# Performance work log

Hardware: AMD Instinct MI355X
Metric: run time of the kernel (lower is better)

Reference implementation:

```python
import jax, jax.numpy as jnp
import numpy as np

N = 50000   # nodes
E = 800000  # edges (before self-loops)
DIN = 128
H, C = 4, 32
HC = H * C  # 128
DE = 3      # edge feature dim
G = 64      # graphs in batch
HID = 32
DOUT = 1
LN_EPS = 1e-5


def setup_inputs() -> dict:
    key = jax.random.key(0)
    ks = iter(jax.random.split(key, 64))
    def nrm(shape, s=0.1):
        return jax.random.normal(next(ks), shape, dtype=jnp.float32) * s
    inp = {}
    inp["x"] = jax.random.normal(next(ks), (N, DIN), dtype=jnp.float32)
    inp["edge_index"] = jax.random.randint(next(ks), (2, E), 0, N, dtype=jnp.int32)
    inp["batch"] = jnp.sort(jax.random.randint(next(ks), (N,), 0, G, dtype=jnp.int32))
    inp["edge_attr"] = jax.random.normal(next(ks), (E, DE), dtype=jnp.float32)
    # GATv2 layers: layer0 in=DIN(128); layers 1,2 in=HC(128)
    for l, din in enumerate([DIN, HC, HC]):
        inp[f"Wl{l}"] = nrm((HC, din)); inp[f"bl{l}"] = jnp.zeros((HC,), jnp.float32)
        inp[f"Wr{l}"] = nrm((HC, din)); inp[f"br{l}"] = jnp.zeros((HC,), jnp.float32)
        inp[f"We{l}"] = nrm((HC, DE))
        inp[f"att{l}"] = nrm((H, C))
        inp[f"bo{l}"] = jnp.zeros((HC,), jnp.float32)
    for l in range(2):
        inp[f"ln{l}_g"] = jnp.ones((HC,), jnp.float32)
        inp[f"ln{l}_b"] = jnp.zeros((HC,), jnp.float32)
    # post-processing MLP: 128->32->32->32->1
    inp["pw1"] = nrm((HID, HC)); inp["pb1"] = jnp.zeros((HID,), jnp.float32)
    inp["pw2"] = nrm((HID, HID)); inp["pb2"] = jnp.zeros((HID,), jnp.float32)
    inp["pw3"] = nrm((HID, HID)); inp["pb3"] = jnp.zeros((HID,), jnp.float32)
    inp["pw4"] = nrm((DOUT, HID)); inp["pb4"] = jnp.zeros((DOUT,), jnp.float32)
    return inp


def _gat_layer(x, src, dst, eattr, Wl, bl, Wr, br, We, att, bo):
    # GATv2Conv (concat heads). x_l from lin_l -> source, x_r from lin_r -> target.
    xl = (x @ Wl.T + bl).reshape(-1, H, C)
    xr = (x @ Wr.T + br).reshape(-1, H, C)
    e = (eattr @ We.T).reshape(-1, H, C)
    m = jax.nn.leaky_relu(xl[src] + xr[dst] + e, negative_slope=0.2)  # [E',H,C]
    s = jnp.einsum('ehc,hc->eh', m, att)                              # [E',H]
    smax = jax.ops.segment_max(s, dst, num_segments=N)
    ex = jnp.exp(s - smax[dst])
    den = jax.ops.segment_sum(ex, dst, num_segments=N)
    alpha = ex / (den[dst] + 1e-16)
    out = jax.ops.segment_sum(alpha[:, :, None] * xl[src], dst, num_segments=N)
    return out.reshape(-1, HC) + bo


def _ln(x, g, b):
    mu = jnp.mean(x, axis=-1, keepdims=True)
    var = jnp.mean((x - mu) ** 2, axis=-1, keepdims=True)
    return (x - mu) * jax.lax.rsqrt(var + LN_EPS) * g + b


def _forward(x, edge_attr, edge_index, batch, p):
    src0, dst0 = edge_index[0], edge_index[1]
    # PyG add_self_loops with fill_value='mean': per-dst-node mean of edge_attr
    cnt = jax.ops.segment_sum(jnp.ones((E,), jnp.float32), dst0, num_segments=N)
    loop_attr = jax.ops.segment_sum(edge_attr, dst0, num_segments=N) / jnp.maximum(cnt, 1.0)[:, None]
    ar = jnp.arange(N, dtype=src0.dtype)
    src = jnp.concatenate([src0, ar]); dst = jnp.concatenate([dst0, ar])
    ea = jnp.concatenate([edge_attr, loop_attr], axis=0)
    embedding = x
    for l in range(3):
        x = _gat_layer(x, src, dst, ea, p[f"Wl{l}"], p[f"bl{l}"], p[f"Wr{l}"],
                       p[f"br{l}"], p[f"We{l}"], p[f"att{l}"], p[f"bo{l}"])
        embedding = x
        x = jax.nn.relu(x)  # dropout inactive (eval)
        if l != 2:
            x = _ln(x, p[f"ln{l}_g"], p[f"ln{l}_b"])
    pooled = jax.ops.segment_max(x, batch, num_segments=G)
    pooled = jnp.where(jnp.isfinite(pooled), pooled, 0.0)
    h = jax.nn.relu(pooled @ p["pw1"].T + p["pb1"])
    h = jax.nn.relu(h @ p["pw2"].T + p["pb2"])
    h = jax.nn.relu(h @ p["pw3"].T + p["pb3"])
    out = h @ p["pw4"].T + p["pb4"]
    return embedding, out


def reference(x, edge_index, batch, edge_attr,
              Wl0, bl0, Wr0, br0, We0, att0, bo0,
              Wl1, bl1, Wr1, br1, We1, att1, bo1,
              Wl2, bl2, Wr2, br2, We2, att2, bo2,
              ln0_g, ln0_b, ln1_g, ln1_b,
              pw1, pb1, pw2, pb2, pw3, pb3, pw4, pb4):
    p = dict(Wl0=Wl0, bl0=bl0, Wr0=Wr0, br0=br0, We0=We0, att0=att0, bo0=bo0,
             Wl1=Wl1, bl1=bl1, Wr1=Wr1, br1=br1, We1=We1, att1=att1, bo1=bo1,
             Wl2=Wl2, bl2=bl2, Wr2=Wr2, br2=br2, We2=We2, att2=att2, bo2=bo2,
             ln0_g=ln0_g, ln0_b=ln0_b, ln1_g=ln1_g, ln1_b=ln1_b,
             pw1=pw1, pb1=pb1, pw2=pw2, pb2=pb2, pw3=pw3, pb3=pb3, pw4=pw4, pb4=pb4)
    return _forward(x, edge_attr, edge_index, batch, p)
```

## Files before the change

### kernel.cpp

```cpp
#include <hip/hip_runtime.h>
#include <math.h>


#define LN_EPS 1e-5f
#define LOG2E 1.44269504088896340736f

typedef short bf16x8 __attribute__((ext_vector_type(8)));
typedef float f32x4 __attribute__((ext_vector_type(4)));

static __device__ __forceinline__ unsigned short f2bf(float f) {
  unsigned int u = __float_as_uint(f);
  u += 0x7fffu + ((u >> 16) & 1u);
  return (unsigned short)(u >> 16);
}

static __device__ __forceinline__ float dpp_sum8(float v) {
  int x;
  x = __builtin_amdgcn_update_dpp(0, __float_as_int(v), 0x0B1, 0xf, 0xf, true);
  v += __int_as_float(x);
  x = __builtin_amdgcn_update_dpp(0, __float_as_int(v), 0x04E, 0xf, 0xf, true);
  v += __int_as_float(x);
  x = __builtin_amdgcn_update_dpp(0, __float_as_int(v), 0x141, 0xf, 0xf, true);
  v += __int_as_float(x);
  return v;
}


__global__ void k_degree(const int* __restrict__ ei, int* __restrict__ cnt, int E) {
  int e = (blockIdx.x * blockDim.x + threadIdx.x) * 4;
  if (e + 3 < E) {
    int4 d = *(const int4*)&ei[E + e];
    atomicAdd(&cnt[d.x], 1);
    atomicAdd(&cnt[d.y], 1);
    atomicAdd(&cnt[d.z], 1);
    atomicAdd(&cnt[d.w], 1);
  } else {
    int lim = min(e + 4, E);
    for (; e < lim; ++e) atomicAdd(&cnt[ei[E + e]], 1);
  }
}

__global__ void k_scan1(const int* __restrict__ cnt, int* __restrict__ bsum, int N) {
  __shared__ int sh[256];
  int t = threadIdx.x;
  int n = blockIdx.x * 256 + t;
  sh[t] = (n < N) ? (cnt[n] + 1) : 0;
  __syncthreads();
  for (int s = 128; s > 0; s >>= 1) {
    if (t < s) sh[t] += sh[t + s];
    __syncthreads();
  }
  if (t == 0) bsum[blockIdx.x] = sh[0];
}

__global__ void k_scan2(int* __restrict__ bsum, int* __restrict__ offs, int nb, int total, int N) {
  __shared__ int sh[256];
  int t = threadIdx.x;
  int v = (t < nb) ? bsum[t] : 0;
  sh[t] = v;
  __syncthreads();
  for (int d = 1; d < 256; d <<= 1) {
    int add = (t >= d) ? sh[t - d] : 0;
    __syncthreads();
    sh[t] += add;
    __syncthreads();
  }
  if (t < nb) bsum[t] = sh[t] - v;
  if (t == 0) offs[N] = total;
}

__global__ void k_scan3(const int* __restrict__ cnt, const int* __restrict__ bsum,
                        int* __restrict__ offs, int* __restrict__ cursor, int N) {
  __shared__ int sh[256];
  int t = threadIdx.x;
  int n = blockIdx.x * 256 + t;
  int v = (n < N) ? (cnt[n] + 1) : 0;
  sh[t] = v;
  __syncthreads();
  for (int d = 1; d < 256; d <<= 1) {
    int add = (t >= d) ? sh[t - d] : 0;
    __syncthreads();
    sh[t] += add;
    __syncthreads();
  }
  if (n < N) {
    int o = bsum[blockIdx.x] + sh[t] - v;
    offs[n] = o;
    cursor[n] = o;
  }
}

__global__ void k_scatter(const int* __restrict__ ei, const float* __restrict__ ea,
                          int* __restrict__ cursor, float4* __restrict__ e4, int E) {
  int e = blockIdx.x * blockDim.x + threadIdx.x;
  if (e >= E) return;
  int s = ei[e];
  int d = ei[E + e];
  int pos = atomicAdd(&cursor[d], 1);
  float4 r;
  r.x = ea[e * 3 + 0];
  r.y = ea[e * 3 + 1];
  r.z = ea[e * 3 + 2];
  r.w = __int_as_float(s * 256);
  e4[pos] = r;
}

__global__ void k_selfloop(const int* __restrict__ offs, float4* __restrict__ e4, int N) {
  int n = blockIdx.x * blockDim.x + threadIdx.x;
  if (n >= N) return;
  int beg = offs[n], last = offs[n + 1] - 1;
  float s0 = 0.f, s1 = 0.f, s2 = 0.f;
  for (int p = beg; p < last; ++p) {
    float4 v = e4[p];
    s0 += v.x;
    s1 += v.y;
    s2 += v.z;
  }
  float invc = 1.0f / fmaxf((float)(last - beg), 1.0f);
  float4 r;
  r.x = s0 * invc;
  r.y = s1 * invc;
  r.z = s2 * invc;
  r.w = __int_as_float(n * 256);
  e4[last] = r;
}


__global__ void k_convx(const float* __restrict__ x, unsigned short* __restrict__ xb, int n) {
  int i = (blockIdx.x * blockDim.x + threadIdx.x) * 4;
  if (i >= n) return;
  float4 v = *(const float4*)&x[i];
  ushort4 o;
  o.x = f2bf(v.x); o.y = f2bf(v.y); o.z = f2bf(v.z); o.w = f2bf(v.w);
  *(ushort4*)&xb[i] = o;
}

__global__ void k_convW(const float* __restrict__ w0, const float* __restrict__ w1,
                        const float* __restrict__ w2, const float* __restrict__ w3,
                        const float* __restrict__ w4, const float* __restrict__ w5,
                        unsigned short* __restrict__ dst) {
  const float* srcs[6] = {w0, w1, w2, w3, w4, w5};
  const float* s = srcs[blockIdx.y];
  int i = blockIdx.x * 256 + threadIdx.x;
  dst[(size_t)blockIdx.y * 16384 + i] = f2bf(s[i]);
}

__global__ __launch_bounds__(256) void k_gemm_mfma(const unsigned short* __restrict__ xb,
                                                   const unsigned short* __restrict__ Wb,
                                                   const float* __restrict__ bl, const float* __restrict__ br,
                                                   unsigned short* __restrict__ xlb,
                                                   unsigned short* __restrict__ xrb, int N) {
  int wave = threadIdx.x >> 6;
  int lane = threadIdx.x & 63;
  int which = blockIdx.y;
  const unsigned short* W = Wb + (size_t)which * 16384;
  const float* bias = which ? br : bl;
  unsigned short* out = which ? xrb : xlb;

  int row0 = (blockIdx.x * 4 + wave) * 16;
  if (row0 >= N) return;
  int m = lane & 15;
  int q = lane >> 4;

  int arow = row0 + m;
  if (arow >= N) arow = N - 1;
  const unsigned short* xrow = xb + (size_t)arow * 128 + q * 8;

  bf16x8 afrag[4];
#pragma unroll
  for (int kt = 0; kt < 4; ++kt) afrag[kt] = *(const bf16x8*)(xrow + kt * 32);

  f32x4 acc[8];
#pragma unroll
  for (int jt = 0; jt < 8; ++jt) acc[jt] = (f32x4){0.f, 0.f, 0.f, 0.f};

  const unsigned short* wbase = W + (size_t)m * 128 + q * 8;
#pragma unroll
  for (int kt = 0; kt < 4; ++kt) {
    bf16x8 a = afrag[kt];
#pragma unroll
    for (int jt = 0; jt < 8; ++jt) {
      bf16x8 b = *(const bf16x8*)(wbase + (size_t)jt * 16 * 128 + kt * 32);
      acc[jt] = __builtin_amdgcn_mfma_f32_16x16x32_bf16(a, b, acc[jt], 0, 0, 0);
    }
  }

#pragma unroll
  for (int jt = 0; jt < 8; ++jt) {
    float bs = bias[jt * 16 + m];
#pragma unroll
    for (int r = 0; r < 4; ++r) {
      int rr = row0 + q * 4 + r;
      if (rr < N) out[(size_t)rr * 128 + jt * 16 + m] = f2bf(acc[jt][r] + bs);
    }
  }
}

__global__ __launch_bounds__(256) void k_agg(const unsigned short* __restrict__ xlb,
                                             const unsigned short* __restrict__ xrb,
                                             const float4* __restrict__ e4,
                                             const int* __restrict__ offs,
                                             const float* __restrict__ We, const float* __restrict__ att,
                                             const float* __restrict__ bo,
                                             const float* __restrict__ lng, const float* __restrict__ lnb,
                                             unsigned short* __restrict__ xnext_bf,
                                             float* __restrict__ emb, int last, int N) {
  int w = (blockIdx.x * blockDim.x + threadIdx.x) >> 6;
  if (w >= N) return;
  int lane = threadIdx.x & 63;
  int half = lane >> 5;
  int sl = lane & 31;
  int c = sl * 4;
  unsigned int c2 = (unsigned int)(c * 2);
  int beg = offs[w], end = offs[w + 1];
  int cnt = end - beg;

  f32x4 xr4, wea, web, wec, at4;
  {
    uint2 vr = *(const uint2*)&xrb[(size_t)w * 128 + c];
    xr4[0] = __uint_as_float(vr.x << 16);
    xr4[1] = __uint_as_float(vr.x & 0xffff0000u);
    xr4[2] = __uint_as_float(vr.y << 16);
    xr4[3] = __uint_as_float(vr.y & 0xffff0000u);
#pragma unroll
    for (int j = 0; j < 4; ++j) {
      wea[j] = We[(c + j) * 3 + 0];
      web[j] = We[(c + j) * 3 + 1];
      wec[j] = We[(c + j) * 3 + 2];
      at4[j] = att[c + j] * LOG2E;
    }
  }

  const char* xlB = (const char*)xlb;
  const char* e4B = (const char*)e4;
  unsigned int lastoff = (unsigned int)(end - 1) << 4;
  unsigned int eoff = (unsigned int)(beg + half) << 4;
  if (eoff > lastoff) eoff = lastoff;

  float l = 0.f;
  f32x4 acc = {0.f, 0.f, 0.f, 0.f};

  int T = (cnt + 1) >> 1;
  float4 eC = *(const float4*)(e4B + eoff);

#pragma unroll 2
  for (int it = 0; it < T - 1; ++it) {
    unsigned int noff = eoff + 32u;
    if (noff > lastoff) noff = lastoff;
    float4 eN = *(const float4*)(e4B + noff);
    eoff = noff;

    unsigned int go = (unsigned int)__float_as_int(eC.w) + c2;
    uint2 v = *(const uint2*)(xlB + go);
    f32x4 xl4;
    xl4[0] = __uint_as_float(v.x << 16);
    xl4[1] = __uint_as_float(v.x & 0xffff0000u);
    xl4[2] = __uint_as_float(v.y << 16);
    xl4[3] = __uint_as_float(v.y & 0xffff0000u);

    f32x4 t = xr4 + wea * eC.x + web * eC.y + wec * eC.z + xl4;
    t[0] = fmaxf(t[0], 0.2f * t[0]);
    t[1] = fmaxf(t[1], 0.2f * t[1]);
    t[2] = fmaxf(t[2], 0.2f * t[2]);
    t[3] = fmaxf(t[3], 0.2f * t[3]);
    float s = t[0] * at4[0] + t[1] * at4[1] + t[2] * at4[2] + t[3] * at4[3];
    float wgt = __builtin_amdgcn_exp2f(dpp_sum8(s));
    l += wgt;
    acc += xl4 * wgt;
    eC = eN;
  }
  {
    int idx = 2 * (T - 1) + half;
    unsigned int go = (unsigned int)__float_as_int(eC.w) + c2;
    uint2 v = *(const uint2*)(xlB + go);
    f32x4 xl4;
    xl4[0] = __uint_as_float(v.x << 16);
    xl4[1] = __uint_as_float(v.x & 0xffff0000u);
    xl4[2] = __uint_as_float(v.y << 16);
    xl4[3] = __uint_as_float(v.y & 0xffff0000u);
    f32x4 t = xr4 + wea * eC.x + web * eC.y + wec * eC.z + xl4;
    t[0] = fmaxf(t[0], 0.2f * t[0]);
    t[1] = fmaxf(t[1], 0.2f * t[1]);
    t[2] = fmaxf(t[2], 0.2f * t[2]);
    t[3] = fmaxf(t[3], 0.2f * t[3]);
    float s = t[0] * at4[0] + t[1] * at4[1] + t[2] * at4[2] + t[3] * at4[3];
    float wgt = __builtin_amdgcn_exp2f(dpp_sum8(s));
    if (idx >= cnt) wgt = 0.f;
    l += wgt;
    acc += xl4 * wgt;
  }

  l += __shfl_xor(l, 32);
  acc[0] += __shfl_xor(acc[0], 32);
  acc[1] += __shfl_xor(acc[1], 32);
  acc[2] += __shfl_xor(acc[2], 32);
  acc[3] += __shfl_xor(acc[3], 32);

  float inv = 1.0f / l;
  f32x4 o;
  const float4 bo4 = *(const float4*)&bo[c];
  o[0] = acc[0] * inv + bo4.x;
  o[1] = acc[1] * inv + bo4.y;
  o[2] = acc[2] * inv + bo4.z;
  o[3] = acc[3] * inv + bo4.w;

  if (last) {
    if (half == 0) {
      float4 st = {o[0], o[1], o[2], o[3]};
      *(float4*)&emb[(size_t)w * 128 + c] = st;
    }
  } else {
    f32x4 r;
    r[0] = fmaxf(o[0], 0.f);
    r[1] = fmaxf(o[1], 0.f);
    r[2] = fmaxf(o[2], 0.f);
    r[3] = fmaxf(o[3], 0.f);
    float s = r[0] + r[1] + r[2] + r[3];
    s += __shfl_xor(s, 1);
    s += __shfl_xor(s, 2);
    s += __shfl_xor(s, 4);
    s += __shfl_xor(s, 8);
    s += __shfl_xor(s, 16);
    float mu = s * 0.0078125f;
    f32x4 d;
    d[0] = r[0] - mu;
    d[1] = r[1] - mu;
    d[2] = r[2] - mu;
    d[3] = r[3] - mu;
    float v2 = d[0] * d[0] + d[1] * d[1] + d[2] * d[2] + d[3] * d[3];
    v2 += __shfl_xor(v2, 1);
    v2 += __shfl_xor(v2, 2);
    v2 += __shfl_xor(v2, 4);
    v2 += __shfl_xor(v2, 8);
    v2 += __shfl_xor(v2, 16);
    float var = v2 * 0.0078125f;
    float rstd = rsqrtf(var + LN_EPS);
    if (half == 0) {
      const float4 g4 = *(const float4*)&lng[c];
      const float4 b4 = *(const float4*)&lnb[c];
      float o0 = d[0] * rstd * g4.x + b4.x;
      float o1 = d[1] * rstd * g4.y + b4.y;
      float o2 = d[2] * rstd * g4.z + b4.z;
      float o3 = d[3] * rstd * g4.w + b4.w;
      uint2 pack;
      pack.x = (unsigned int)f2bf(o0) | ((unsigned int)f2bf(o1) << 16);
      pack.y = (unsigned int)f2bf(o2) | ((unsigned int)f2bf(o3) << 16);
      *(uint2*)&xnext_bf[(size_t)w * 128 + c] = pack;
    }
  }
}

__global__ void k_pool(const float* __restrict__ emb, const int* __restrict__ batch,
                       float* __restrict__ pooled, int N) {
  int c = threadIdx.x & 127;
  int half = threadIdx.x >> 7;
  int base = blockIdx.x * 64 + half;
  int limit = min(blockIdx.x * 64 + 64, N);
  float cur = 0.f;
  int curg = -1;
  for (int n = base; n < limit; n += 2) {
    int g = batch[n];
    if (g != curg) {
      if (curg >= 0) atomicMax((unsigned int*)&pooled[curg * 128 + c], __float_as_uint(cur));
      curg = g;
      cur = 0.f;
    }
    cur = fmaxf(cur, emb[(size_t)n * 128 + c]);
  }
  if (curg >= 0) atomicMax((unsigned int*)&pooled[curg * 128 + c], __float_as_uint(cur));
}

__global__ void k_mlp(const float* __restrict__ pooled,
                      const float* __restrict__ pw1, const float* __restrict__ pb1,
                      const float* __restrict__ pw2, const float* __restrict__ pb2,
                      const float* __restrict__ pw3, const float* __restrict__ pb3,
                      const float* __restrict__ pw4, const float* __restrict__ pb4,
                      float* __restrict__ out) {
  int g = blockIdx.x;
  int t = threadIdx.x;
  __shared__ float buf1[32], buf2[32];
  if (t < 32) {
    float acc = pb1[t];
    for (int k = 0; k < 128; ++k) acc += pw1[t * 128 + k] * pooled[g * 128 + k];
    buf1[t] = fmaxf(acc, 0.f);
  }
  __syncthreads();
  if (t < 32) {
    float acc = pb2[t];
    for (int k = 0; k < 32; ++k) acc += pw2[t * 32 + k] * buf1[k];
    buf2[t] = fmaxf(acc, 0.f);
  }
  __syncthreads();
  if (t < 32) {
    float acc = pb3[t];
    for (int k = 0; k < 32; ++k) acc += pw3[t * 32 + k] * buf2[k];
    buf1[t] = fmaxf(acc, 0.f);
  }
  __syncthreads();
  if (t == 0) {
    float acc = pb4[0];
    for (int k = 0; k < 32; ++k) acc += pw4[k] * buf1[k];
    out[g] = acc;
  }
}


extern "C" void kernel_launch(void* const* d_in, const int* in_sizes, int n_in,
                              void* d_out, int out_size, void* d_ws, size_t ws_size,
                              hipStream_t stream) {
  const float* x_in = (const float*)d_in[0];
  const int* ei = (const int*)d_in[1];
  const int* batch = (const int*)d_in[2];
  const float* ea = (const float*)d_in[3];

  const int N = in_sizes[0] / 128;
  const int E = in_sizes[1] / 2;
  const int EP = E + N;
  const int G = out_size - N * 128;

  const float *Wl[3], *bl[3], *Wr[3], *br[3], *We[3], *att[3], *bo[3];
  for (int l = 0; l < 3; ++l) {
    Wl[l] = (const float*)d_in[4 + 7 * l];
    bl[l] = (const float*)d_in[5 + 7 * l];
    Wr[l] = (const float*)d_in[6 + 7 * l];
    br[l] = (const float*)d_in[7 + 7 * l];
    We[l] = (const float*)d_in[8 + 7 * l];
    att[l] = (const float*)d_in[9 + 7 * l];
    bo[l] = (const float*)d_in[10 + 7 * l];
  }
  const float* lng[2] = {(const float*)d_in[25], (const float*)d_in[27]};
  const float* lnb[2] = {(const float*)d_in[26], (const float*)d_in[28]};
  const float* pw1 = (const float*)d_in[29];
  const float* pb1 = (const float*)d_in[30];
  const float* pw2 = (const float*)d_in[31];
  const float* pb2 = (const float*)d_in[32];
  const float* pw3 = (const float*)d_in[33];
  const float* pb3 = (const float*)d_in[34];
  const float* pw4 = (const float*)d_in[35];
  const float* pb4 = (const float*)d_in[36];

  char* base = (char*)d_ws;
  size_t cur = 0;
  auto carve = [&](size_t bytes) -> char* {
    char* p = base + cur;
    cur += (bytes + 255) & ~(size_t)255;
    return p;
  };
  unsigned short* xlb = (unsigned short*)carve((size_t)N * 128 * 2);
  unsigned short* xrb = (unsigned short*)carve((size_t)N * 128 * 2);
  unsigned short* xb = (unsigned short*)carve((size_t)N * 128 * 2);
  unsigned short* Wb = (unsigned short*)carve((size_t)6 * 16384 * 2);
  float4* e4 = (float4*)carve((size_t)EP * 16);
  int* offs = (int*)carve((size_t)(N + 1) * 4);
  int* cursor = (int*)carve((size_t)N * 4);
  int* cnt = (int*)carve((size_t)N * 4);
  int* bsum = (int*)carve(1024);
  float* pooled = (float*)carve((size_t)G * 128 * 4);

  float* emb_out = (float*)d_out;
  float* mlp_out = (float*)d_out + (size_t)N * 128;

  const int NB = (N + 255) / 256;

  hipMemsetAsync(cnt, 0, (size_t)N * 4, stream);
  hipMemsetAsync(pooled, 0, (size_t)G * 128 * 4, stream);

  k_degree<<<(E / 4 + 255) / 256, 256, 0, stream>>>(ei, cnt, E);
  k_scan1<<<NB, 256, 0, stream>>>(cnt, bsum, N);
  k_scan2<<<1, 256, 0, stream>>>(bsum, offs, NB, EP, N);
  k_scan3<<<NB, 256, 0, stream>>>(cnt, bsum, offs, cursor, N);
  k_scatter<<<(E + 255) / 256, 256, 0, stream>>>(ei, ea, cursor, e4, E);
  k_selfloop<<<NB, 256, 0, stream>>>(offs, e4, N);

  k_convx<<<(N * 128 / 4 + 255) / 256, 256, 0, stream>>>(x_in, xb, N * 128);
  {
    dim3 g(64, 6);
    k_convW<<<g, 256, 0, stream>>>(Wl[0], Wr[0], Wl[1], Wr[1], Wl[2], Wr[2], Wb);
  }

  for (int l = 0; l < 3; ++l) {
    dim3 ggrid((N + 63) / 64, 2);
    k_gemm_mfma<<<ggrid, 256, 0, stream>>>(xb, Wb + (size_t)l * 32768, bl[l], br[l], xlb, xrb, N);
    int last = (l == 2) ? 1 : 0;
    const float* g = last ? bo[l] : lng[l];
    const float* b = last ? bo[l] : lnb[l];
    k_agg<<<(N * 64 + 255) / 256, 256, 0, stream>>>(xlb, xrb, e4, offs,
                                                    We[l], att[l], bo[l], g, b,
                                                    xb, emb_out, last, N);
  }

  k_pool<<<(N + 63) / 64, 256, 0, stream>>>(emb_out, batch, pooled, N);
  k_mlp<<<G, 64, 0, stream>>>(pooled, pw1, pb1, pw2, pb2, pw3, pb3, pw4, pb4, mlp_out);
}
```

Baseline: 554.9 us.

## Replace global-atomic CSR scatter with two-pass bucketed binning and parallel self-loop

The per-edge global atomicAdd scatter into destination-sorted order is replaced by two passes. First, each block builds a shared-memory histogram of destination buckets (256 nodes each), reserves space with one global atomic per bucket, and writes edges into a staging buffer. Second, each bucket is scattered to final positions using shared-memory atomics. The self-loop mean kernel now uses 4 threads per node with shuffle reductions. The aim is less global atomic contention and better write locality, at the cost of an extra staging buffer, one more pass over the edge records, and packing src/dst into 16 bits each, which assumes N < 65536.

```diff
diff --git a/kernel.cpp b/kernel.cpp
--- a/kernel.cpp
+++ b/kernel.cpp
@@ -70,7 +70,7 @@
 }
 
 __global__ void k_scan3(const int* __restrict__ cnt, const int* __restrict__ bsum,
-                        int* __restrict__ offs, int* __restrict__ cursor, int N) {
+                        int* __restrict__ offs, int N) {
   __shared__ int sh[256];
   int t = threadIdx.x;
   int n = blockIdx.x * 256 + t;
@@ -83,46 +83,107 @@
     sh[t] += add;
     __syncthreads();
   }
-  if (n < N) {
-    int o = bsum[blockIdx.x] + sh[t] - v;
-    offs[n] = o;
-    cursor[n] = o;
-  }
-}
-
-__global__ void k_scatter(const int* __restrict__ ei, const float* __restrict__ ea,
-                          int* __restrict__ cursor, float4* __restrict__ e4, int E) {
-  int e = blockIdx.x * blockDim.x + threadIdx.x;
-  if (e >= E) return;
-  int s = ei[e];
-  int d = ei[E + e];
-  int pos = atomicAdd(&cursor[d], 1);
-  float4 r;
-  r.x = ea[e * 3 + 0];
-  r.y = ea[e * 3 + 1];
-  r.z = ea[e * 3 + 2];
-  r.w = __int_as_float(s * 256);
-  e4[pos] = r;
+  if (n < N) offs[n] = bsum[blockIdx.x] + sh[t] - v;
+}
+
+__global__ void k_initcur(const int* __restrict__ offs, int* __restrict__ gcur, int nbuk) {
+  int t = threadIdx.x;
+  if (t < nbuk) gcur[t] = offs[t * 256];
+}
+
+#define CHUNK 4096
+__global__ __launch_bounds__(256) void k_binA(const int* __restrict__ ei, const float* __restrict__ ea,
+                                              int* __restrict__ gcur, float4* __restrict__ staged,
+                                              int E, int nbuk) {
+  __shared__ int hist[256];
+  __shared__ int basebuf[256];
+  int t = threadIdx.x;
+  int e0 = blockIdx.x * CHUNK;
+
+  hist[t] = 0;
+  __syncthreads();
+#pragma unroll
+  for (int i = 0; i < CHUNK / 256; ++i) {
+    int e = e0 + i * 256 + t;
+    if (e < E) atomicAdd(&hist[ei[E + e] >> 8], 1);
+  }
+  __syncthreads();
+  int h = hist[t];
+  if (t < nbuk && h > 0) basebuf[t] = atomicAdd(&gcur[t], h);
+  hist[t] = 0;
+  __syncthreads();
+#pragma unroll
+  for (int i = 0; i < CHUNK / 256; ++i) {
+    int e = e0 + i * 256 + t;
+    if (e < E) {
+      int s = ei[e];
+      int d = ei[E + e];
+      int b = d >> 8;
+      int r = atomicAdd(&hist[b], 1);
+      float4 rec;
+      rec.x = ea[e * 3 + 0];
+      rec.y = ea[e * 3 + 1];
+      rec.z = ea[e * 3 + 2];
+      rec.w = __int_as_float(s | (d << 16));
+      staged[basebuf[b] + r] = rec;
+    }
+  }
+}
+
+__global__ __launch_bounds__(256) void k_binB(const float4* __restrict__ staged,
+                                              const int* __restrict__ offs,
+                                              float4* __restrict__ e4, int N) {
+  __shared__ int cur[256];
+  int t = threadIdx.x;
+  int n0 = blockIdx.x * 256;
+  int n1 = min(n0 + 256, N);
+  if (n0 + t < n1) cur[t] = offs[n0 + t];
+  int start = offs[n0];
+  int cntReal = (offs[n1] - start) - (n1 - n0);
+  __syncthreads();
+  for (int p = start + t; p < start + cntReal; p += 256) {
+    float4 rec = staged[p];
+    unsigned int u = (unsigned int)__float_as_int(rec.w);
+    int s = (int)(u & 0xffffu);
+    int d = (int)(u >> 16);
+    int pos = atomicAdd(&cur[d - n0], 1);
+    float4 out;
+    out.x = rec.x;
+    out.y = rec.y;
+    out.z = rec.z;
+    out.w = __int_as_float(s * 256);
+    e4[pos] = out;
+  }
 }
 
 __global__ void k_selfloop(const int* __restrict__ offs, float4* __restrict__ e4, int N) {
-  int n = blockIdx.x * blockDim.x + threadIdx.x;
+  int idx = blockIdx.x * blockDim.x + threadIdx.x;
+  int n = idx >> 2;
   if (n >= N) return;
+  int sub = idx & 3;
   int beg = offs[n], last = offs[n + 1] - 1;
   float s0 = 0.f, s1 = 0.f, s2 = 0.f;
-  for (int p = beg; p < last; ++p) {
+  for (int p = beg + sub; p < last; p += 4) {
     float4 v = e4[p];
     s0 += v.x;
     s1 += v.y;
     s2 += v.z;
   }
-  float invc = 1.0f / fmaxf((float)(last - beg), 1.0f);
-  float4 r;
-  r.x = s0 * invc;
-  r.y = s1 * invc;
-  r.z = s2 * invc;
-  r.w = __int_as_float(n * 256);
-  e4[last] = r;
+  s0 += __shfl_xor(s0, 1);
+  s1 += __shfl_xor(s1, 1);
+  s2 += __shfl_xor(s2, 1);
+  s0 += __shfl_xor(s0, 2);
+  s1 += __shfl_xor(s1, 2);
+  s2 += __shfl_xor(s2, 2);
+  if (sub == 0) {
+    float invc = 1.0f / fmaxf((float)(last - beg), 1.0f);
+    float4 r;
+    r.x = s0 * invc;
+    r.y = s1 * invc;
+    r.z = s2 * invc;
+    r.w = __int_as_float(n * 256);
+    e4[last] = r;
+  }
 }
 
 
@@ -417,6 +478,7 @@
   const int E = in_sizes[1] / 2;
   const int EP = E + N;
   const int G = out_size - N * 128;
+  const int NBUK = (N + 255) / 256;
 
   const float *Wl[3], *bl[3], *Wr[3], *br[3], *We[3], *att[3], *bo[3];
   for (int l = 0; l < 3; ++l) {
@@ -451,9 +513,10 @@
   unsigned short* xb = (unsigned short*)carve((size_t)N * 128 * 2);
   unsigned short* Wb = (unsigned short*)carve((size_t)6 * 16384 * 2);
   float4* e4 = (float4*)carve((size_t)EP * 16);
+  float4* staged = (float4*)carve((size_t)EP * 16);
   int* offs = (int*)carve((size_t)(N + 1) * 4);
-  int* cursor = (int*)carve((size_t)N * 4);
   int* cnt = (int*)carve((size_t)N * 4);
+  int* gcur = (int*)carve((size_t)(NBUK + 1) * 4);
   int* bsum = (int*)carve(1024);
   float* pooled = (float*)carve((size_t)G * 128 * 4);
 
@@ -468,9 +531,11 @@
   k_degree<<<(E / 4 + 255) / 256, 256, 0, stream>>>(ei, cnt, E);
   k_scan1<<<NB, 256, 0, stream>>>(cnt, bsum, N);
   k_scan2<<<1, 256, 0, stream>>>(bsum, offs, NB, EP, N);
-  k_scan3<<<NB, 256, 0, stream>>>(cnt, bsum, offs, cursor, N);
-  k_scatter<<<(E + 255) / 256, 256, 0, stream>>>(ei, ea, cursor, e4, E);
-  k_selfloop<<<NB, 256, 0, stream>>>(offs, e4, N);
+  k_scan3<<<NB, 256, 0, stream>>>(cnt, bsum, offs, N);
+  k_initcur<<<1, 256, 0, stream>>>(offs, gcur, NBUK);
+  k_binA<<<(E + CHUNK - 1) / CHUNK, 256, 0, stream>>>(ei, ea, gcur, staged, E, NBUK);
+  k_binB<<<NBUK, 256, 0, stream>>>(staged, offs, e4, N);
+  k_selfloop<<<(N * 4 + 255) / 256, 256, 0, stream>>>(offs, e4, N);
 
   k_convx<<<(N * 128 / 4 + 255) / 256, 256, 0, stream>>>(x_in, xb, N * 128);
   {
```

Measured after the change: 530.2 us. -4.4%, faster.
